# Kernel tuning notes

Measured on AMD Instinct MI355X. Metric: run time of the kernel, lower is better.

Reference implementation:

```python
import jax, jax.numpy as jnp
import numpy as np

M, B, S, D = 3, 8, 512, 768
NORM = 1.0 / np.sqrt(D)


def setup_inputs() -> dict:
    key = jax.random.key(0)
    ks = jax.random.split(key, 5)
    modality = jax.random.normal(ks[0], (M, B, S, D), dtype=jnp.float32)
    # per-modality projection Linear(D, D): y = x @ W.T + b
    Wp = jax.random.normal(ks[1], (M, D, D), dtype=jnp.float32) * (1.0 / np.sqrt(D))
    bp = jax.random.normal(ks[2], (M, D), dtype=jnp.float32) * 0.01
    # confidence Linear(D, S)
    Wc = jax.random.normal(ks[3], (S, D), dtype=jnp.float32) * (1.0 / np.sqrt(D))
    bc = jax.random.normal(ks[4], (S,), dtype=jnp.float32) * 0.01
    return {"modality": modality, "Wp": Wp, "bp": bp, "Wc": Wc, "bc": bc}


def reference(modality, Wp, bp, Wc, bc):
    m, b, s, d = modality.shape
    norm = jnp.asarray(NORM, modality.dtype)
    # per-modality projection + relu: [M,B,S,D]
    proj = jax.nn.relu(jnp.einsum('mbsd,med->mbse', modality, Wp) + bp[:, None, None, :])
    # pairwise scores: i = query modality, j = key modality -> [M,M,B,S,S]
    scores = jax.nn.relu(jnp.einsum('ibsd,jbtd->ijbst', proj, proj) * norm)
    scores = jax.nn.softmax(scores, axis=-1)
    # values per pair: scores[i,j] @ proj[j] -> [M,M,B,S,D]
    values = jnp.einsum('ijbst,jbtd->ijbsd', scores, proj)
    # sum of per-query score stacks: sum_i scores[i] -> [M,B,S,S]
    attn_scores_sum = jnp.sum(scores, axis=0)
    # confidence: sigmoid(Linear(D,S)(proj)) -> [M,B,S,S]
    confidence = jax.nn.sigmoid(jnp.einsum('mbsd,td->mbst', proj, Wc) + bc)
    gca_loss = jnp.mean((attn_scores_sum - confidence) ** 2)
    # final combine: matmul(scores, values) over last two dims -> [M,M,B,S,D]
    out = jnp.einsum('ijbst,ijbtd->ijbsd', scores, values)
    out = out.reshape(b, m * m * s * d)
    return gca_loss, out
```

## Files before the change

kernel.cpp:

```cpp
#include <hip/hip_runtime.h>
#include <hip/hip_bf16.h>

typedef __bf16 bf16_t;
typedef __bf16 bf16x8 __attribute__((ext_vector_type(8)));
typedef float f32x4 __attribute__((ext_vector_type(4)));

static constexpr int Mm = 3, Bb = 8, Ss = 512, Dd = 768;
static constexpr float NORMF = 0.036084391824351615f;

#define BM 128
#define BN 128
#define BK 32
#define NT 256

enum { EPI_PROJ = 0, EPI_E, EPI_CONF, EPI_BF16, EPI_F32 };

__device__ __forceinline__ void gload16(const void* g, void* l) {
#if defined(__has_builtin) && __has_builtin(__builtin_amdgcn_global_load_lds)
    __builtin_amdgcn_global_load_lds(
        (const __attribute__((address_space(1))) void*)g,
        (__attribute__((address_space(3))) void*)l, 16, 0, 0);
#else
    *(bf16x8*)l = *(const bf16x8*)g;
#endif
}

template<int NXY, int NX>
__device__ __forceinline__ void decode_swz(int& bx, int& by, int& bz) {
    const int bid = blockIdx.x;
    const int q = gridDim.x >> 3;
    const int wid = (bid & 7) * q + (bid >> 3);
    bz = wid / NXY;
    const int rem = wid - bz * NXY;
    by = rem / NX;
    bx = rem - by * NX;
}

template<int EPI, bool F32IN>
__device__ __forceinline__ void gemm_core(
    const void* __restrict__ Ap, const void* __restrict__ Bp,
    int lda, int ldb, int K,
    void* __restrict__ Cp, int ldc,
    const float* __restrict__ bias, float scale,
    int rowBase, int colBase)
{
    __shared__ bf16_t As[BM][BK];
    __shared__ bf16_t Bs[BN][BK];

    const int tid  = threadIdx.x;
    const int lane = tid & 63;
    const int wv   = tid >> 6;
    const int wr   = wv >> 1, wc = wv & 1;
    const int lg   = lane >> 4, l16 = lane & 15;

    f32x4 acc[4][4] = {};

    const int nk = K / BK;
    for (int kt = 0; kt < nk; ++kt) {
        __syncthreads();
        const int gk = kt * BK;
        if (F32IN) {
            #pragma unroll
            for (int it = 0; it < 2; ++it) {
                const int c  = tid + it * NT;
                const int r  = c >> 2;
                const int k8 = (c & 3) * 8;
                const float* sa = (const float*)Ap + (size_t)(rowBase + r) * lda + gk + k8;
                const f32x4 a0 = *(const f32x4*)sa;
                const f32x4 a1 = *(const f32x4*)(sa + 4);
                bf16x8 v;
                #pragma unroll
                for (int q = 0; q < 4; ++q) { v[q] = (bf16_t)a0[q]; v[q + 4] = (bf16_t)a1[q]; }
                *(bf16x8*)&As[r][k8] = v;
                const float* sb = (const float*)Bp + (size_t)(colBase + r) * ldb + gk + k8;
                const f32x4 b0 = *(const f32x4*)sb;
                const f32x4 b1 = *(const f32x4*)(sb + 4);
                bf16x8 w;
                #pragma unroll
                for (int q = 0; q < 4; ++q) { w[q] = (bf16_t)b0[q]; w[q + 4] = (bf16_t)b1[q]; }
                *(bf16x8*)&Bs[r][k8] = w;
            }
        } else {
            #pragma unroll
            for (int it = 0; it < 2; ++it) {
                const int c  = tid + it * NT;
                const int r  = c >> 2;
                const int k8 = (c & 3) * 8;
                const bf16_t* ga = (const bf16_t*)Ap + (size_t)(rowBase + r) * lda + gk + k8;
                gload16(ga, (char*)As + (size_t)(wv * 64 + it * NT) * 16);
                const bf16_t* gb = (const bf16_t*)Bp + (size_t)(colBase + r) * ldb + gk + k8;
                gload16(gb, (char*)Bs + (size_t)(wv * 64 + it * NT) * 16);
            }
            asm volatile("s_waitcnt vmcnt(0)" ::: "memory");
            __builtin_amdgcn_sched_barrier(0);
        }
        __syncthreads();

        bf16x8 af[4], bfr[4];
        #pragma unroll
        for (int m = 0; m < 4; ++m)
            af[m] = *(const bf16x8*)&As[wr * 64 + m * 16 + l16][lg * 8];
        #pragma unroll
        for (int n = 0; n < 4; ++n)
            bfr[n] = *(const bf16x8*)&Bs[wc * 64 + n * 16 + l16][lg * 8];
        #pragma unroll
        for (int m = 0; m < 4; ++m)
            #pragma unroll
            for (int n = 0; n < 4; ++n)
                acc[m][n] = __builtin_amdgcn_mfma_f32_16x16x32_bf16(af[m], bfr[n], acc[m][n], 0, 0, 0);
    }

    #pragma unroll
    for (int m = 0; m < 4; ++m) {
        #pragma unroll
        for (int n = 0; n < 4; ++n) {
            #pragma unroll
            for (int r = 0; r < 4; ++r) {
                const int row = rowBase + wr * 64 + m * 16 + lg * 4 + r;
                const int col = colBase + wc * 64 + n * 16 + l16;
                float v = acc[m][n][r];
                if (EPI == EPI_PROJ) {
                    v = fmaxf(v + bias[col], 0.f);
                    ((bf16_t*)Cp)[(size_t)row * ldc + col] = (bf16_t)v;
                } else if (EPI == EPI_E) {
                    v = fmaxf(v * scale, 0.f);
                    ((bf16_t*)Cp)[(size_t)row * ldc + col] = (bf16_t)v;
                } else if (EPI == EPI_CONF) {
                    v = v + bias[col];
                    v = 1.f / (1.f + __expf(-v));
                    ((bf16_t*)Cp)[(size_t)row * ldc + col] = (bf16_t)v;
                } else if (EPI == EPI_BF16) {
                    ((bf16_t*)Cp)[(size_t)row * ldc + col] = (bf16_t)v;
                } else {
                    ((float*)Cp)[(size_t)row * ldc + col] = v;
                }
            }
        }
    }
}


__global__ __launch_bounds__(NT) void k_proj(const float* __restrict__ mod,
                                             const float* __restrict__ Wp,
                                             const float* __restrict__ bp,
                                             bf16_t* __restrict__ proj) {
    int bx, by, m;
    decode_swz<192, 6>(bx, by, m);
    gemm_core<EPI_PROJ, true>(
        mod + (size_t)m * Bb * Ss * Dd, Wp + (size_t)m * Dd * Dd, Dd, Dd, Dd,
        proj + (size_t)m * Bb * Ss * Dd, Dd, bp + m * Dd, 1.f,
        by * BM, bx * BN);
}

__global__ __launch_bounds__(NT) void k_scores(const bf16_t* __restrict__ proj,
                                               bf16_t* __restrict__ E) {
    int bx, by, z;
    decode_swz<16, 4>(bx, by, z);
    const int i = z / 24, j = (z / 8) % 3, b = z % 8;
    gemm_core<EPI_E, false>(
        proj + (size_t)(i * Bb + b) * Ss * Dd,
        proj + (size_t)(j * Bb + b) * Ss * Dd, Dd, Dd, Dd,
        E + (size_t)z * Ss * Ss, Ss, nullptr, NORMF,
        by * BM, bx * BN);
}

__global__ __launch_bounds__(NT) void k_conf(const bf16_t* __restrict__ proj,
                                             const bf16_t* __restrict__ wcbf,
                                             const float* __restrict__ bc,
                                             bf16_t* __restrict__ conf) {
    int bx, by, z;
    decode_swz<16, 4>(bx, by, z);
    gemm_core<EPI_CONF, false>(
        proj + (size_t)z * Ss * Dd, wcbf, Dd, Dd, Dd,
        conf + (size_t)z * Ss * Ss, Ss, bc, 1.f,
        by * BM, bx * BN);
}

__global__ __launch_bounds__(NT) void k_s2(const bf16_t* __restrict__ P,
                                           const bf16_t* __restrict__ Pt,
                                           bf16_t* __restrict__ s2) {
    int bx, by, z;
    decode_swz<16, 4>(bx, by, z);
    const size_t SS = (size_t)Ss * Ss;
    gemm_core<EPI_BF16, false>(
        P + (size_t)z * SS, Pt + (size_t)z * SS, Ss, Ss, Ss,
        s2 + (size_t)z * SS, Ss, nullptr, 1.f,
        by * BM, bx * BN);
}

__global__ __launch_bounds__(NT) void k_out(const bf16_t* __restrict__ s2,
                                            const bf16_t* __restrict__ projT,
                                            float* __restrict__ outp) {
    int bx, by, z;
    decode_swz<24, 6>(bx, by, z);
    const int j = (z / 8) % 3, b = z % 8;
    gemm_core<EPI_F32, false>(
        s2 + (size_t)z * Ss * Ss,
        projT + (size_t)(j * Bb + b) * Dd * Ss, Ss, Ss, Ss,
        outp + (size_t)z * Ss * Dd, Dd, nullptr, 1.f,
        by * BM, bx * BN);
}

__global__ __launch_bounds__(NT) void k_transpose(const bf16_t* __restrict__ in,
                                                  bf16_t* __restrict__ out,
                                                  int R, int C) {
    __shared__ bf16_t t[64][80];
    const size_t z = blockIdx.z;
    const bf16_t* ip = in + z * (size_t)R * C;
    bf16_t* op = out + z * (size_t)R * C;
    const int r0 = blockIdx.y * 64, c0 = blockIdx.x * 64;
    const int tid = threadIdx.x;
    #pragma unroll
    for (int it = 0; it < 2; ++it) {
        const int c = tid + it * NT;
        const int r = c >> 3, cc = (c & 7) * 8;
        *(bf16x8*)&t[r][cc] = *(const bf16x8*)(ip + (size_t)(r0 + r) * C + c0 + cc);
    }
    __syncthreads();
    #pragma unroll
    for (int it = 0; it < 2; ++it) {
        const int c = tid + it * NT;
        const int oc = c >> 3, rr = (c & 7) * 8;
        bf16x8 v;
        #pragma unroll
        for (int k = 0; k < 8; ++k) v[k] = t[rr + k][oc];
        *(bf16x8*)(op + (size_t)(c0 + oc) * R + r0 + rr) = v;
    }
}

__device__ __forceinline__ int lidx(int r, int c) {
    int cb = (c >> 3) ^ (r & 7) ^ ((r >> 3) & 7);
    return r * 512 + cb * 8 + (c & 7);
}

__global__ __launch_bounds__(NT) void k_softmaxT(const bf16_t* __restrict__ E,
                                                 bf16_t* __restrict__ P,
                                                 bf16_t* __restrict__ Pt) {
    __shared__ bf16_t L[64 * 512];
    const int z = blockIdx.y, strip = blockIdx.x;
    const size_t SS = (size_t)Ss * Ss;
    const bf16_t* ep = E + (size_t)z * SS + (size_t)strip * 64 * Ss;
    const int tid = threadIdx.x, lane = tid & 63, wv = tid >> 6;

    #pragma unroll 4
    for (int rr = 0; rr < 16; ++rr) {
        const int r = wv * 16 + rr;
        const bf16x8 v8 = *(const bf16x8*)(ep + (size_t)r * Ss + lane * 8);
        float v[8];
        float mx = -1e30f;
        #pragma unroll
        for (int q = 0; q < 8; ++q) { v[q] = (float)v8[q]; mx = fmaxf(mx, v[q]); }
        #pragma unroll
        for (int off = 1; off < 64; off <<= 1) mx = fmaxf(mx, __shfl_xor(mx, off, 64));
        float e[8], s = 0.f;
        #pragma unroll
        for (int q = 0; q < 8; ++q) { e[q] = __expf(v[q] - mx); s += e[q]; }
        #pragma unroll
        for (int off = 1; off < 64; off <<= 1) s += __shfl_xor(s, off, 64);
        const float inv = 1.f / s;
        bf16x8 o;
        #pragma unroll
        for (int q = 0; q < 8; ++q) o[q] = (bf16_t)(e[q] * inv);
        *(bf16x8*)&L[lidx(r, lane * 8)] = o;
    }
    __syncthreads();

    bf16_t* pp = P + (size_t)z * SS + (size_t)strip * 64 * Ss;
    #pragma unroll
    for (int k = 0; k < 16; ++k) {
        const int cc = tid + k * NT;
        const int r = cc >> 6, c8 = (cc & 63) * 8;
        *(bf16x8*)(pp + (size_t)r * Ss + c8) = *(const bf16x8*)&L[lidx(r, c8)];
    }
    bf16_t* pt = Pt + (size_t)z * SS + strip * 64;
    #pragma unroll
    for (int k = 0; k < 16; ++k) {
        const int cc = tid + k * NT;
        const int t = cc >> 3, s8 = (cc & 7) * 8;
        bf16x8 o;
        #pragma unroll
        for (int q = 0; q < 8; ++q) o[q] = L[lidx(s8 + q, t)];
        *(bf16x8*)(pt + (size_t)t * Ss + s8) = o;
    }
}

__global__ void k_init(const float* __restrict__ Wc, bf16_t* __restrict__ wcbf,
                       float* __restrict__ out0) {
    const int i = blockIdx.x * NT + threadIdx.x;
    if (i == 0) out0[0] = 0.f;
    if (i < Ss * Dd) wcbf[i] = (bf16_t)Wc[i];
}

__global__ __launch_bounds__(NT) void k_loss(const bf16_t* __restrict__ P,
                                             const bf16_t* __restrict__ conf,
                                             float* __restrict__ out0) {
    const size_t NE = (size_t)Mm * Bb * Ss * Ss;
    const size_t NCH = NE / 8;
    float local = 0.f;
    for (size_t c = blockIdx.x * (size_t)NT + threadIdx.x; c < NCH;
         c += gridDim.x * (size_t)NT) {
        const size_t base = c * 8;
        const bf16x8 s0 = *(const bf16x8*)(P + base);
        const bf16x8 s1 = *(const bf16x8*)(P + base + NE);
        const bf16x8 s2 = *(const bf16x8*)(P + base + 2 * NE);
        const bf16x8 cf = *(const bf16x8*)(conf + base);
        #pragma unroll
        for (int k = 0; k < 8; ++k) {
            const float d = (float)s0[k] + (float)s1[k] + (float)s2[k] - (float)cf[k];
            local += d * d;
        }
    }
    #pragma unroll
    for (int off = 1; off < 64; off <<= 1) local += __shfl_xor(local, off, 64);
    __shared__ float wsum[4];
    if ((threadIdx.x & 63) == 0) wsum[threadIdx.x >> 6] = local;
    __syncthreads();
    if (threadIdx.x == 0) {
        const float s = wsum[0] + wsum[1] + wsum[2] + wsum[3];
        atomicAdd(out0, s * (1.0f / (float)NE));
    }
}


extern "C" void kernel_launch(void* const* d_in, const int* in_sizes, int n_in,
                              void* d_out, int out_size, void* d_ws, size_t ws_size,
                              hipStream_t stream) {
    const float* modality = (const float*)d_in[0];
    const float* Wp = (const float*)d_in[1];
    const float* bp = (const float*)d_in[2];
    const float* Wc = (const float*)d_in[3];
    const float* bc = (const float*)d_in[4];
    float* out = (float*)d_out;

    char* ws = (char*)d_ws;
    bf16_t* proj  = (bf16_t*)(ws + 0);
    bf16_t* projT = (bf16_t*)(ws + 18874368);
    bf16_t* wcbf  = (bf16_t*)(ws + 37748736);
    bf16_t* P     = (bf16_t*)(ws + 38535168);
    bf16_t* Pt    = (bf16_t*)(ws + 76283904);
    bf16_t* E     = (bf16_t*)(ws + 114032640);
    bf16_t* S2    = (bf16_t*)(ws + 114032640);
    bf16_t* conf  = (bf16_t*)(ws + 151781376);

    k_init<<<dim3((Ss * Dd) / NT), NT, 0, stream>>>(Wc, wcbf, out);
    k_proj<<<dim3(576), NT, 0, stream>>>(modality, Wp, bp, proj);
    k_transpose<<<dim3(Dd / 64, Ss / 64, Mm * Bb), NT, 0, stream>>>(proj, projT, Ss, Dd);
    k_scores<<<dim3(1152), NT, 0, stream>>>(proj, E);
    k_softmaxT<<<dim3(Ss / 64, Mm * Mm * Bb), NT, 0, stream>>>(E, P, Pt);
    k_conf<<<dim3(384), NT, 0, stream>>>(proj, wcbf, bc, conf);
    k_s2<<<dim3(1152), NT, 0, stream>>>(P, Pt, S2);
    k_out<<<dim3(1728), NT, 0, stream>>>(S2, projT, out + 1);
    k_loss<<<dim3(1024), NT, 0, stream>>>(P, conf, out);
}
```

Measured before the change: 379.0 us.

## Replace GEMM core with 256x256 8-wave pipelined multi-buffered LDS kernel

Replaces the 128x128 single-stage GEMM core with a 256x256 tile, 512-thread core. It uses an 8-slot LDS ring with prefetch of seven stages ahead, XOR-swizzled LDS layout, and fine-grained barriers with setprio around the MFMA blocks. Inputs are converted to bf16 in a separate prep kernel so the projection GEMM can also use direct global-to-LDS loads. Scores and confidence GEMMs are merged into one launch. This aims to hide memory latency and raise MFMA utilisation, at the cost of large LDS use (128KB per block), fewer blocks for the projection (144 on a 256-CU part), and an extra fp32 to bf16 conversion pass.

Measured after the change: 394.4 us. 1.04x slower.

```diff
diff --git a/kernel.cpp b/kernel.cpp
--- a/kernel.cpp
+++ b/kernel.cpp
@@ -8,131 +8,130 @@
 static constexpr int Mm = 3, Bb = 8, Ss = 512, Dd = 768;
 static constexpr float NORMF = 0.036084391824351615f;
 
-#define BM 128
-#define BN 128
-#define BK 32
-#define NT 256
-
 enum { EPI_PROJ = 0, EPI_E, EPI_CONF, EPI_BF16, EPI_F32 };
 
 __device__ __forceinline__ void gload16(const void* g, void* l) {
-#if defined(__has_builtin) && __has_builtin(__builtin_amdgcn_global_load_lds)
     __builtin_amdgcn_global_load_lds(
         (const __attribute__((address_space(1))) void*)g,
         (__attribute__((address_space(3))) void*)l, 16, 0, 0);
-#else
-    *(bf16x8*)l = *(const bf16x8*)g;
-#endif
-}
-
-template<int NXY, int NX>
-__device__ __forceinline__ void decode_swz(int& bx, int& by, int& bz) {
-    const int bid = blockIdx.x;
-    const int q = gridDim.x >> 3;
-    const int wid = (bid & 7) * q + (bid >> 3);
-    bz = wid / NXY;
-    const int rem = wid - bz * NXY;
-    by = rem / NX;
-    bx = rem - by * NX;
-}
-
-template<int EPI, bool F32IN>
-__device__ __forceinline__ void gemm_core(
-    const void* __restrict__ Ap, const void* __restrict__ Bp,
-    int lda, int ldb, int K,
-    void* __restrict__ Cp, int ldc,
+}
+
+#define FENCE() do { asm volatile("" ::: "memory"); __builtin_amdgcn_sched_barrier(0); } while (0)
+#define BARRIER() do { FENCE(); __builtin_amdgcn_s_barrier(); FENCE(); } while (0)
+
+typedef bf16_t ldsrow_t[8192];
+
+template<int EPI, int K>
+__device__ __forceinline__ void gemm8_core(
+    ldsrow_t* __restrict__ lds,
+    const bf16_t* __restrict__ Ap, const bf16_t* __restrict__ Bp,
+    int lda, int ldb, void* __restrict__ Cp, int ldc,
     const float* __restrict__ bias, float scale,
     int rowBase, int colBase)
 {
-    __shared__ bf16_t As[BM][BK];
-    __shared__ bf16_t Bs[BN][BK];
-
-    const int tid  = threadIdx.x;
-    const int lane = tid & 63;
-    const int wv   = tid >> 6;
-    const int wr   = wv >> 1, wc = wv & 1;
-    const int lg   = lane >> 4, l16 = lane & 15;
-
-    f32x4 acc[4][4] = {};
-
-    const int nk = K / BK;
-    for (int kt = 0; kt < nk; ++kt) {
-        __syncthreads();
-        const int gk = kt * BK;
-        if (F32IN) {
-            #pragma unroll
-            for (int it = 0; it < 2; ++it) {
-                const int c  = tid + it * NT;
-                const int r  = c >> 2;
-                const int k8 = (c & 3) * 8;
-                const float* sa = (const float*)Ap + (size_t)(rowBase + r) * lda + gk + k8;
-                const f32x4 a0 = *(const f32x4*)sa;
-                const f32x4 a1 = *(const f32x4*)(sa + 4);
-                bf16x8 v;
-                #pragma unroll
-                for (int q = 0; q < 4; ++q) { v[q] = (bf16_t)a0[q]; v[q + 4] = (bf16_t)a1[q]; }
-                *(bf16x8*)&As[r][k8] = v;
-                const float* sb = (const float*)Bp + (size_t)(colBase + r) * ldb + gk + k8;
-                const f32x4 b0 = *(const f32x4*)sb;
-                const f32x4 b1 = *(const f32x4*)(sb + 4);
-                bf16x8 w;
-                #pragma unroll
-                for (int q = 0; q < 4; ++q) { w[q] = (bf16_t)b0[q]; w[q + 4] = (bf16_t)b1[q]; }
-                *(bf16x8*)&Bs[r][k8] = w;
-            }
-        } else {
-            #pragma unroll
-            for (int it = 0; it < 2; ++it) {
-                const int c  = tid + it * NT;
-                const int r  = c >> 2;
-                const int k8 = (c & 3) * 8;
-                const bf16_t* ga = (const bf16_t*)Ap + (size_t)(rowBase + r) * lda + gk + k8;
-                gload16(ga, (char*)As + (size_t)(wv * 64 + it * NT) * 16);
-                const bf16_t* gb = (const bf16_t*)Bp + (size_t)(colBase + r) * ldb + gk + k8;
-                gload16(gb, (char*)Bs + (size_t)(wv * 64 + it * NT) * 16);
-            }
-            asm volatile("s_waitcnt vmcnt(0)" ::: "memory");
-            __builtin_amdgcn_sched_barrier(0);
-        }
-        __syncthreads();
-
-        bf16x8 af[4], bfr[4];
-        #pragma unroll
-        for (int m = 0; m < 4; ++m)
-            af[m] = *(const bf16x8*)&As[wr * 64 + m * 16 + l16][lg * 8];
-        #pragma unroll
-        for (int n = 0; n < 4; ++n)
-            bfr[n] = *(const bf16x8*)&Bs[wc * 64 + n * 16 + l16][lg * 8];
-        #pragma unroll
-        for (int m = 0; m < 4; ++m)
-            #pragma unroll
-            for (int n = 0; n < 4; ++n)
-                acc[m][n] = __builtin_amdgcn_mfma_f32_16x16x32_bf16(af[m], bfr[n], acc[m][n], 0, 0, 0);
-    }
-
-    #pragma unroll
-    for (int m = 0; m < 4; ++m) {
-        #pragma unroll
-        for (int n = 0; n < 4; ++n) {
+    constexpr int NKT = K / 64;
+
+    const int tid = threadIdx.x, lane = tid & 63, wv = tid >> 6;
+    const int wr = wv >> 2, wc = wv & 3;
+    const int lg = lane >> 4, l16 = lane & 15;
+    const int swz8 = (lg ^ ((l16 >> 1) & 3)) * 8;
+
+    f32x4 acc[8][4] = {};
+    bf16x8 af[4], bfr[4];
+
+#define STAGE(hh) do {                                                        \
+    const int t_  = ((hh) >> 2) % NKT;                                        \
+    const int p_  = (hh) & 3;                                                 \
+    const int sl_ = (((hh) >> 2) & 1) * 4 + p_;                               \
+    const bf16_t* s_ = (p_ & 1) ? Ap : Bp;                                    \
+    const int ld_ = (p_ & 1) ? lda : ldb;                                     \
+    const int rb_ = (p_ & 1) ? rowBase : colBase;                             \
+    const int kb_ = t_ * 64 + (p_ >> 1) * 32;                                 \
+    _Pragma("unroll")                                                         \
+    for (int q_ = 0; q_ < 2; ++q_) {                                          \
+        const int row_ = (wv * 2 + q_) * 16 + (lane >> 2);                    \
+        const int ck_  = (lane & 3) ^ ((row_ >> 1) & 3);                      \
+        gload16(s_ + (size_t)(rb_ + row_) * ld_ + kb_ + ck_ * 8,              \
+                (char*)&lds[sl_][0] + (wv * 2 + q_) * 1024);                  \
+    }                                                                         \
+} while (0)
+
+#define RD_A(sl_, rh_) do {                                                   \
+    _Pragma("unroll")                                                         \
+    for (int rf_ = 0; rf_ < 4; ++rf_)                                         \
+        af[rf_] = *(const bf16x8*)&lds[sl_][(wr*128 + (rh_)*64 + rf_*16 + l16)*32 + swz8]; \
+} while (0)
+
+#define RD_B(sl_) do {                                                        \
+    _Pragma("unroll")                                                         \
+    for (int cf_ = 0; cf_ < 4; ++cf_)                                         \
+        bfr[cf_] = *(const bf16x8*)&lds[sl_][(wc*64 + cf_*16 + l16)*32 + swz8]; \
+} while (0)
+
+#define PHASE(bb_, ks_, rh_, LAST_) do {                                      \
+    if (rh_ == 0) RD_B((bb_)*4 + (ks_)*2);                                    \
+    RD_A((bb_)*4 + (ks_)*2 + 1, rh_);                                         \
+    STAGE(h); ++h;                                                            \
+    BARRIER();                                                                \
+    asm volatile("s_waitcnt lgkmcnt(0)" ::: "memory");                        \
+    __builtin_amdgcn_sched_barrier(0);                                        \
+    __builtin_amdgcn_s_setprio(1);                                            \
+    _Pragma("unroll")                                                         \
+    for (int rf_ = 0; rf_ < 4; ++rf_) {                                       \
+        _Pragma("unroll")                                                     \
+        for (int cf_ = 0; cf_ < 4; ++cf_)                                     \
+            acc[(rh_)*4 + rf_][cf_] = __builtin_amdgcn_mfma_f32_16x16x32_bf16( \
+                af[rf_], bfr[cf_], acc[(rh_)*4 + rf_][cf_], 0, 0, 0);         \
+    }                                                                         \
+    __builtin_amdgcn_s_setprio(0);                                            \
+    if (LAST_) { asm volatile("s_waitcnt vmcnt(6)" ::: "memory"); }           \
+    BARRIER();                                                                \
+} while (0)
+
+    int h = 0;
+    #pragma unroll
+    for (int p = 0; p < 7; ++p) { STAGE(h); ++h; }
+    asm volatile("s_waitcnt vmcnt(6)" ::: "memory");
+    BARRIER();
+
+    for (int it = 0; it < NKT / 2; ++it) {
+        PHASE(0, 0, 0, false); PHASE(0, 0, 1, false);
+        PHASE(0, 1, 0, false); PHASE(0, 1, 1, true);
+        PHASE(1, 0, 0, false); PHASE(1, 0, 1, false);
+        PHASE(1, 1, 0, false); PHASE(1, 1, 1, true);
+    }
+
+    asm volatile("s_waitcnt vmcnt(0)" ::: "memory");
+    __builtin_amdgcn_sched_barrier(0);
+
+#undef PHASE
+#undef RD_A
+#undef RD_B
+#undef STAGE
+
+    #pragma unroll
+    for (int cf = 0; cf < 4; ++cf) {
+        const int gc = colBase + wc * 64 + cf * 16 + l16;
+        const float bv = (EPI == EPI_PROJ || EPI == EPI_CONF) ? bias[gc] : 0.f;
+        #pragma unroll
+        for (int rg = 0; rg < 8; ++rg) {
             #pragma unroll
             for (int r = 0; r < 4; ++r) {
-                const int row = rowBase + wr * 64 + m * 16 + lg * 4 + r;
-                const int col = colBase + wc * 64 + n * 16 + l16;
-                float v = acc[m][n][r];
+                const int gr = rowBase + wr * 128 + rg * 16 + lg * 4 + r;
+                float v = acc[rg][cf][r];
                 if (EPI == EPI_PROJ) {
-                    v = fmaxf(v + bias[col], 0.f);
-                    ((bf16_t*)Cp)[(size_t)row * ldc + col] = (bf16_t)v;
+                    v = fmaxf(v + bv, 0.f);
+                    ((bf16_t*)Cp)[(size_t)gr * ldc + gc] = (bf16_t)v;
                 } else if (EPI == EPI_E) {
                     v = fmaxf(v * scale, 0.f);
-                    ((bf16_t*)Cp)[(size_t)row * ldc + col] = (bf16_t)v;
+                    ((bf16_t*)Cp)[(size_t)gr * ldc + gc] = (bf16_t)v;
                 } else if (EPI == EPI_CONF) {
-                    v = v + bias[col];
-                    v = 1.f / (1.f + __expf(-v));
-                    ((bf16_t*)Cp)[(size_t)row * ldc + col] = (bf16_t)v;
+                    v = 1.f / (1.f + __expf(-(v + bv)));
+                    ((bf16_t*)Cp)[(size_t)gr * ldc + gc] = (bf16_t)v;
                 } else if (EPI == EPI_BF16) {
-                    ((bf16_t*)Cp)[(size_t)row * ldc + col] = (bf16_t)v;
+                    ((bf16_t*)Cp)[(size_t)gr * ldc + gc] = (bf16_t)v;
                 } else {
-                    ((float*)Cp)[(size_t)row * ldc + col] = v;
+                    ((float*)Cp)[(size_t)gr * ldc + gc] = v;
                 }
             }
         }
@@ -140,70 +139,78 @@
 }
 
 
-__global__ __launch_bounds__(NT) void k_proj(const float* __restrict__ mod,
-                                             const float* __restrict__ Wp,
-                                             const float* __restrict__ bp,
-                                             bf16_t* __restrict__ proj) {
-    int bx, by, m;
-    decode_swz<192, 6>(bx, by, m);
-    gemm_core<EPI_PROJ, true>(
-        mod + (size_t)m * Bb * Ss * Dd, Wp + (size_t)m * Dd * Dd, Dd, Dd, Dd,
+__device__ __forceinline__ int xcd_swz(int n) {
+    return (blockIdx.x & 7) * (n >> 3) + (blockIdx.x >> 3);
+}
+
+__global__ __launch_bounds__(512) void k_proj8(const bf16_t* __restrict__ modB,
+                                               const bf16_t* __restrict__ WpB,
+                                               const float* __restrict__ bp,
+                                               bf16_t* __restrict__ proj) {
+    __shared__ bf16_t lds[8][8192];
+    const int wid = xcd_swz(144);
+    const int m = wid / 48, rem = wid % 48;
+    const int by = rem / 3, bx = rem % 3;
+    gemm8_core<EPI_PROJ, 768>(lds,
+        modB + (size_t)m * Bb * Ss * Dd, WpB + (size_t)m * Dd * Dd, Dd, Dd,
         proj + (size_t)m * Bb * Ss * Dd, Dd, bp + m * Dd, 1.f,
-        by * BM, bx * BN);
-}
-
-__global__ __launch_bounds__(NT) void k_scores(const bf16_t* __restrict__ proj,
-                                               bf16_t* __restrict__ E) {
-    int bx, by, z;
-    decode_swz<16, 4>(bx, by, z);
-    const int i = z / 24, j = (z / 8) % 3, b = z % 8;
-    gemm_core<EPI_E, false>(
-        proj + (size_t)(i * Bb + b) * Ss * Dd,
-        proj + (size_t)(j * Bb + b) * Ss * Dd, Dd, Dd, Dd,
-        E + (size_t)z * Ss * Ss, Ss, nullptr, NORMF,
-        by * BM, bx * BN);
-}
-
-__global__ __launch_bounds__(NT) void k_conf(const bf16_t* __restrict__ proj,
-                                             const bf16_t* __restrict__ wcbf,
-                                             const float* __restrict__ bc,
-                                             bf16_t* __restrict__ conf) {
-    int bx, by, z;
-    decode_swz<16, 4>(bx, by, z);
-    gemm_core<EPI_CONF, false>(
-        proj + (size_t)z * Ss * Dd, wcbf, Dd, Dd, Dd,
-        conf + (size_t)z * Ss * Ss, Ss, bc, 1.f,
-        by * BM, bx * BN);
-}
-
-__global__ __launch_bounds__(NT) void k_s2(const bf16_t* __restrict__ P,
-                                           const bf16_t* __restrict__ Pt,
-                                           bf16_t* __restrict__ s2) {
-    int bx, by, z;
-    decode_swz<16, 4>(bx, by, z);
+        by * 256, bx * 256);
+}
+
+__global__ __launch_bounds__(512) void k_scoresconf(const bf16_t* __restrict__ proj,
+                                                    const bf16_t* __restrict__ wcbf,
+                                                    const float* __restrict__ bc,
+                                                    bf16_t* __restrict__ E,
+                                                    bf16_t* __restrict__ conf) {
+    __shared__ bf16_t lds[8][8192];
+    const int wid = xcd_swz(384);
     const size_t SS = (size_t)Ss * Ss;
-    gemm_core<EPI_BF16, false>(
-        P + (size_t)z * SS, Pt + (size_t)z * SS, Ss, Ss, Ss,
-        s2 + (size_t)z * SS, Ss, nullptr, 1.f,
-        by * BM, bx * BN);
-}
-
-__global__ __launch_bounds__(NT) void k_out(const bf16_t* __restrict__ s2,
-                                            const bf16_t* __restrict__ projT,
-                                            float* __restrict__ outp) {
-    int bx, by, z;
-    decode_swz<24, 6>(bx, by, z);
+    if (wid < 288) {
+        const int z = wid >> 2, q = wid & 3;
+        const int i = z / 24, j = (z / 8) % 3, b = z % 8;
+        gemm8_core<EPI_E, 768>(lds,
+            proj + (size_t)(i * Bb + b) * Ss * Dd,
+            proj + (size_t)(j * Bb + b) * Ss * Dd, Dd, Dd,
+            E + z * SS, Ss, nullptr, NORMF, (q >> 1) * 256, (q & 1) * 256);
+    } else {
+        const int w2 = wid - 288;
+        const int z = w2 >> 2, q = w2 & 3;
+        gemm8_core<EPI_CONF, 768>(lds,
+            proj + (size_t)z * Ss * Dd, wcbf, Dd, Dd,
+            conf + z * SS, Ss, bc, 1.f, (q >> 1) * 256, (q & 1) * 256);
+    }
+}
+
+__global__ __launch_bounds__(512) void k_s28(const bf16_t* __restrict__ P,
+                                             const bf16_t* __restrict__ Pt,
+                                             bf16_t* __restrict__ S2) {
+    __shared__ bf16_t lds[8][8192];
+    const int wid = xcd_swz(288);
+    const int z = wid >> 2, q = wid & 3;
+    const size_t SS = (size_t)Ss * Ss;
+    gemm8_core<EPI_BF16, 512>(lds,
+        P + z * SS, Pt + z * SS, Ss, Ss,
+        S2 + z * SS, Ss, nullptr, 1.f, (q >> 1) * 256, (q & 1) * 256);
+}
+
+__global__ __launch_bounds__(512) void k_out8(const bf16_t* __restrict__ S2,
+                                              const bf16_t* __restrict__ projT,
+                                              float* __restrict__ outp) {
+    __shared__ bf16_t lds[8][8192];
+    const int wid = xcd_swz(432);
+    const int z = wid / 6, q = wid % 6;
     const int j = (z / 8) % 3, b = z % 8;
-    gemm_core<EPI_F32, false>(
-        s2 + (size_t)z * Ss * Ss,
-        projT + (size_t)(j * Bb + b) * Dd * Ss, Ss, Ss, Ss,
+    gemm8_core<EPI_F32, 512>(lds,
+        S2 + (size_t)z * Ss * Ss,
+        projT + (size_t)(j * Bb + b) * Dd * Ss, Ss, Ss,
         outp + (size_t)z * Ss * Dd, Dd, nullptr, 1.f,
-        by * BM, bx * BN);
-}
-
-__global__ __launch_bounds__(NT) void k_transpose(const bf16_t* __restrict__ in,
-                                                  bf16_t* __restrict__ out,
-                                                  int R, int C) {
+        (q / 3) * 256, (q % 3) * 256);
+}
+
+
+__global__ __launch_bounds__(256) void k_transpose(const bf16_t* __restrict__ in,
+                                                   bf16_t* __restrict__ out,
+                                                   int R, int C) {
     __shared__ bf16_t t[64][80];
     const size_t z = blockIdx.z;
     const bf16_t* ip = in + z * (size_t)R * C;
@@ -212,14 +219,14 @@
     const int tid = threadIdx.x;
     #pragma unroll
     for (int it = 0; it < 2; ++it) {
-        const int c = tid + it * NT;
+        const int c = tid + it * 256;
         const int r = c >> 3, cc = (c & 7) * 8;
         *(bf16x8*)&t[r][cc] = *(const bf16x8*)(ip + (size_t)(r0 + r) * C + c0 + cc);
     }
     __syncthreads();
     #pragma unroll
     for (int it = 0; it < 2; ++it) {
-        const int c = tid + it * NT;
+        const int c = tid + it * 256;
         const int oc = c >> 3, rr = (c & 7) * 8;
         bf16x8 v;
         #pragma unroll
@@ -233,9 +240,9 @@
     return r * 512 + cb * 8 + (c & 7);
 }
 
-__global__ __launch_bounds__(NT) void k_softmaxT(const bf16_t* __restrict__ E,
-                                                 bf16_t* __restrict__ P,
-                                                 bf16_t* __restrict__ Pt) {
+__global__ __launch_bounds__(256) void k_softmaxT(const bf16_t* __restrict__ E,
+                                                  bf16_t* __restrict__ P,
+                                                  bf16_t* __restrict__ Pt) {
     __shared__ bf16_t L[64 * 512];
     const int z = blockIdx.y, strip = blockIdx.x;
     const size_t SS = (size_t)Ss * Ss;
@@ -268,14 +275,14 @@
     bf16_t* pp = P + (size_t)z * SS + (size_t)strip * 64 * Ss;
     #pragma unroll
     for (int k = 0; k < 16; ++k) {
-        const int cc = tid + k * NT;
+        const int cc = tid + k * 256;
         const int r = cc >> 6, c8 = (cc & 63) * 8;
         *(bf16x8*)(pp + (size_t)r * Ss + c8) = *(const bf16x8*)&L[lidx(r, c8)];
     }
     bf16_t* pt = Pt + (size_t)z * SS + strip * 64;
     #pragma unroll
     for (int k = 0; k < 16; ++k) {
-        const int cc = tid + k * NT;
+        const int cc = tid + k * 256;
         const int t = cc >> 3, s8 = (cc & 7) * 8;
         bf16x8 o;
         #pragma unroll
@@ -284,21 +291,35 @@
     }
 }
 
-__global__ void k_init(const float* __restrict__ Wc, bf16_t* __restrict__ wcbf,
-                       float* __restrict__ out0) {
-    const int i = blockIdx.x * NT + threadIdx.x;
-    if (i == 0) out0[0] = 0.f;
-    if (i < Ss * Dd) wcbf[i] = (bf16_t)Wc[i];
-}
-
-__global__ __launch_bounds__(NT) void k_loss(const bf16_t* __restrict__ P,
-                                             const bf16_t* __restrict__ conf,
-                                             float* __restrict__ out0) {
+__global__ __launch_bounds__(256) void k_prep(const float* __restrict__ mod,
+                                              const float* __restrict__ Wp,
+                                              const float* __restrict__ Wc,
+                                              bf16_t* __restrict__ modB,
+                                              bf16_t* __restrict__ WpB,
+                                              bf16_t* __restrict__ wcbf,
+                                              float* __restrict__ out0) {
+    const int c = blockIdx.x * 256 + threadIdx.x;
+    if (c == 0) out0[0] = 0.f;
+    const float* src; bf16_t* dst; size_t off;
+    if (c < 1179648)       { src = mod; dst = modB; off = (size_t)c * 8; }
+    else if (c < 1400832)  { src = Wp;  dst = WpB;  off = (size_t)(c - 1179648) * 8; }
+    else                   { src = Wc;  dst = wcbf; off = (size_t)(c - 1400832) * 8; }
+    const f32x4 a = *(const f32x4*)(src + off);
+    const f32x4 b = *(const f32x4*)(src + off + 4);
+    bf16x8 v;
+    #pragma unroll
+    for (int q = 0; q < 4; ++q) { v[q] = (bf16_t)a[q]; v[q + 4] = (bf16_t)b[q]; }
+    *(bf16x8*)(dst + off) = v;
+}
+
+__global__ __launch_bounds__(256) void k_loss(const bf16_t* __restrict__ P,
+                                              const bf16_t* __restrict__ conf,
+                                              float* __restrict__ out0) {
     const size_t NE = (size_t)Mm * Bb * Ss * Ss;
     const size_t NCH = NE / 8;
     float local = 0.f;
-    for (size_t c = blockIdx.x * (size_t)NT + threadIdx.x; c < NCH;
-         c += gridDim.x * (size_t)NT) {
+    for (size_t c = blockIdx.x * (size_t)256 + threadIdx.x; c < NCH;
+         c += gridDim.x * (size_t)256) {
         const size_t base = c * 8;
         const bf16x8 s0 = *(const bf16x8*)(P + base);
         const bf16x8 s1 = *(const bf16x8*)(P + base + NE);
@@ -333,22 +354,23 @@
     float* out = (float*)d_out;
 
     char* ws = (char*)d_ws;
-    bf16_t* proj  = (bf16_t*)(ws + 0);
-    bf16_t* projT = (bf16_t*)(ws + 18874368);
-    bf16_t* wcbf  = (bf16_t*)(ws + 37748736);
-    bf16_t* P     = (bf16_t*)(ws + 38535168);
-    bf16_t* Pt    = (bf16_t*)(ws + 76283904);
-    bf16_t* E     = (bf16_t*)(ws + 114032640);
-    bf16_t* S2    = (bf16_t*)(ws + 114032640);
-    bf16_t* conf  = (bf16_t*)(ws + 151781376);
-
-    k_init<<<dim3((Ss * Dd) / NT), NT, 0, stream>>>(Wc, wcbf, out);
-    k_proj<<<dim3(576), NT, 0, stream>>>(modality, Wp, bp, proj);
-    k_transpose<<<dim3(Dd / 64, Ss / 64, Mm * Bb), NT, 0, stream>>>(proj, projT, Ss, Dd);
-    k_scores<<<dim3(1152), NT, 0, stream>>>(proj, E);
-    k_softmaxT<<<dim3(Ss / 64, Mm * Mm * Bb), NT, 0, stream>>>(E, P, Pt);
-    k_conf<<<dim3(384), NT, 0, stream>>>(proj, wcbf, bc, conf);
-    k_s2<<<dim3(1152), NT, 0, stream>>>(P, Pt, S2);
-    k_out<<<dim3(1728), NT, 0, stream>>>(S2, projT, out + 1);
-    k_loss<<<dim3(1024), NT, 0, stream>>>(P, conf, out);
-}
+    bf16_t* modB  = (bf16_t*)(ws + 0);
+    bf16_t* WpB   = (bf16_t*)(ws + 18874368);
+    bf16_t* wcbf  = (bf16_t*)(ws + 22413312);
+    bf16_t* proj  = (bf16_t*)(ws + 23199744);
+    bf16_t* projT = (bf16_t*)(ws + 42074112);
+    bf16_t* P     = (bf16_t*)(ws + 60948480);
+    bf16_t* Pt    = (bf16_t*)(ws + 98697216);
+    bf16_t* E     = (bf16_t*)(ws + 136445952);
+    bf16_t* S2    = (bf16_t*)(ws + 136445952);
+    bf16_t* conf  = (bf16_t*)(ws + 174194688);
+
+    k_prep<<<dim3(5664), 256, 0, stream>>>(modality, Wp, Wc, modB, WpB, wcbf, out);
+    k_proj8<<<dim3(144), 512, 0, stream>>>(modB, WpB, bp, proj);
+    k_transpose<<<dim3(Dd / 64, Ss / 64, Mm * Bb), 256, 0, stream>>>(proj, projT, Ss, Dd);
+    k_scoresconf<<<dim3(384), 512, 0, stream>>>(proj, wcbf, bc, E, conf);
+    k_softmaxT<<<dim3(Ss / 64, Mm * Mm * Bb), 256, 0, stream>>>(E, P, Pt);
+    k_s28<<<dim3(288), 512, 0, stream>>>(P, Pt, S2);
+    k_out8<<<dim3(432), 512, 0, stream>>>(S2, projT, out + 1);
+    k_loss<<<dim3(1024), 256, 0, stream>>>(P, conf, out);
+}
```
